# Kernel optimization log

Measured on AMD Instinct MI355X. Metric: run time of the kernel, lower is better.

## Reference

```python
import jax, jax.numpy as jnp
import numpy as np

N, M, CIN, COUT, K, KS = 200000, 100000, 32, 64, 32, 3


def setup_inputs() -> dict:
    key = jax.random.key(0)
    ks = jax.random.split(key, 6)
    inp_positions = jax.random.uniform(ks[0], (N, 3), dtype=jnp.float32)
    out_positions = jax.random.uniform(ks[1], (M, 3), dtype=jnp.float32)
    inp_features = jax.random.normal(ks[2], (N, CIN), dtype=jnp.float32)
    inp_importance = jnp.ones((N,), dtype=jnp.float32)
    neighbors_index = jax.random.randint(ks[3], (M, K), 0, N, dtype=jnp.int32)
    kernel = 0.05 * jax.random.normal(ks[4], (KS, KS, KS, CIN, COUT), dtype=jnp.float32)
    bias = jnp.zeros((COUT,), dtype=jnp.float32)
    extents = jnp.ones((1,), dtype=jnp.float32)
    return dict(inp_features=inp_features, inp_positions=inp_positions,
                out_positions=out_positions, extents=extents,
                inp_importance=inp_importance, neighbors_index=neighbors_index,
                kernel=kernel, bias=bias)


def _axis_weights(x):
    """x: [...,] coord clamped to [0, KS-1]. Returns [..., KS] linear interp weights."""
    grid = jnp.arange(KS, dtype=x.dtype)
    return jnp.maximum(0.0, 1.0 - jnp.abs(x[..., None] - grid))


def reference(inp_features, inp_positions, out_positions, extents,
              inp_importance, neighbors_index, kernel, bias):
    radius = 0.5 * extents[0]
    nbr_pos = inp_positions[neighbors_index]                   # [M,K,3]
    rel = (nbr_pos - out_positions[:, None, :]) / radius       # unit-ball coords
    dist = jnp.sqrt(jnp.sum(rel * rel, axis=-1))               # [M,K] L2 metric
    mask = (dist <= 1.0).astype(inp_features.dtype)            # in-radius validity
    # ball_to_cube_radial: scale radially so sphere boundary -> cube boundary
    linf = jnp.max(jnp.abs(rel), axis=-1)                      # [M,K]
    scale = jnp.where(linf > 1e-8, dist / jnp.maximum(linf, 1e-8), 0.0)
    cube = rel * scale[..., None]                              # in [-1,1]^3
    # align_corners=True: map [-1,1] to voxel-center coords [0, KS-1]
    coords = jnp.clip((cube + 1.0) * (0.5 * (KS - 1)), 0.0, KS - 1.0)  # 'linear' clamp
    wx = _axis_weights(coords[..., 0])                         # [M,K,3]
    wy = _axis_weights(coords[..., 1])
    wz = _axis_weights(coords[..., 2])
    imp = mask * inp_importance[neighbors_index]               # [M,K]
    feat = inp_features[neighbors_index] * imp[..., None]      # [M,K,CIN]
    # accumulate importance*interp-weighted features per filter voxel
    acc = jnp.einsum('mka,mkb,mkc,mki->mabci', wx, wy, wz, feat)  # [M,3,3,3,CIN]
    out = jnp.einsum('mabci,abcio->mo', acc, kernel)           # [M,COUT]
    # normalize=True, no window fn -> divide by (importance-weighted) neighbor count
    norm = jnp.sum(imp, axis=1)                                # [M]
    out = out * jnp.where(norm > 0, 1.0 / jnp.maximum(norm, 1e-12), 0.0)[:, None]
    return out + bias  # activation=None
```

## Files before the change

kernel.cpp:

```cpp
#include <hip/hip_runtime.h>


typedef __attribute__((ext_vector_type(8))) __bf16 bf16x8;
typedef __attribute__((ext_vector_type(4))) __bf16 bf16x4;
typedef __attribute__((ext_vector_type(4))) float f32x4;

constexpr int MPTS = 100000;
constexpr int MB   = 8;
constexpr int NBLK = MPTS / MB;

constexpr int PT_STRIDE = 2240;
constexpr int W_V       = 80;
constexpr int NRM_OFF   = MB * PT_STRIDE;
constexpr int LDS_BYTES = NRM_OFF + 32 + 304;

__global__ void wprep_kernel(const float* __restrict__ kern, __bf16* __restrict__ wsb) {
    const int tid = blockIdx.x * 256 + threadIdx.x;
    if (tid >= 4 * 28 * 64 * 8) return;
    const int j  = tid & 7;
    const int l  = (tid >> 3) & 63;
    const int s  = tid >> 9;
    const int ks = s % 28;
    const int nt = s / 28;
    const int kk = ks * 32 + ((l >> 4) << 3) + j;
    const int ch = kk / 28;
    const int v  = kk - ch * 28;
    const int o  = nt * 16 + (l & 15);
    const float val = (v < 27) ? kern[v * 2048 + ch * 64 + o] : 0.0f;
    wsb[tid] = (__bf16)val;
}

#define STAGE(f, A, B) do {                                              \
    f[0]  = feats[(size_t)(A).x * 32 + lr];                              \
    f[1]  = feats[(size_t)(A).y * 32 + lr];                              \
    f[2]  = feats[(size_t)(A).z * 32 + lr];                              \
    f[3]  = feats[(size_t)(A).w * 32 + lr];                              \
    f[4]  = feats[(size_t)(B).x * 32 + lr];                              \
    f[5]  = feats[(size_t)(B).y * 32 + lr];                              \
    f[6]  = feats[(size_t)(B).z * 32 + lr];                              \
    f[7]  = feats[(size_t)(B).w * 32 + lr];                              \
    f[8]  = feats[(size_t)(A).x * 32 + 16 + lr];                         \
    f[9]  = feats[(size_t)(A).y * 32 + 16 + lr];                         \
    f[10] = feats[(size_t)(A).z * 32 + 16 + lr];                         \
    f[11] = feats[(size_t)(A).w * 32 + 16 + lr];                         \
    f[12] = feats[(size_t)(B).x * 32 + 16 + lr];                         \
    f[13] = feats[(size_t)(B).y * 32 + 16 + lr];                         \
    f[14] = feats[(size_t)(B).z * 32 + 16 + lr];                         \
    f[15] = feats[(size_t)(B).w * 32 + 16 + lr];                         \
} while (0)

#define COMPUTE(qq, f) do {                                              \
    unsigned char* pbase = smem + (wv * 4 + (qq)) * PT_STRIDE;           \
    bf16x8 b0, b1;                                                       \
    b0[0] = (__bf16)f[0];  b0[1] = (__bf16)f[1];                         \
    b0[2] = (__bf16)f[2];  b0[3] = (__bf16)f[3];                         \
    b0[4] = (__bf16)f[4];  b0[5] = (__bf16)f[5];                         \
    b0[6] = (__bf16)f[6];  b0[7] = (__bf16)f[7];                         \
    b1[0] = (__bf16)f[8];  b1[1] = (__bf16)f[9];                         \
    b1[2] = (__bf16)f[10]; b1[3] = (__bf16)f[11];                        \
    b1[4] = (__bf16)f[12]; b1[5] = (__bf16)f[13];                        \
    b1[6] = (__bf16)f[14]; b1[7] = (__bf16)f[15];                        \
    const bf16x8 a0 = *(const bf16x8*)(pbase + lr * W_V + k0 * 2);       \
    const bf16x8 a1 = *(const bf16x8*)(pbase + (16 + lr) * W_V + k0 * 2);\
    f32x4 d00 = {0.f,0.f,0.f,0.f}, d01 = {0.f,0.f,0.f,0.f};              \
    f32x4 d10 = {0.f,0.f,0.f,0.f}, d11 = {0.f,0.f,0.f,0.f};              \
    d00 = __builtin_amdgcn_mfma_f32_16x16x32_bf16(a0, b0, d00, 0, 0, 0); \
    d01 = __builtin_amdgcn_mfma_f32_16x16x32_bf16(a0, b1, d01, 0, 0, 0); \
    d10 = __builtin_amdgcn_mfma_f32_16x16x32_bf16(a1, b0, d10, 0, 0, 0); \
    d11 = __builtin_amdgcn_mfma_f32_16x16x32_bf16(a1, b1, d11, 0, 0, 0); \
    const int vb0 = grp * 4, vb1 = 16 + grp * 4;                         \
    bf16x4 t0, t1;                                                       \
    t0[0] = (__bf16)d00[0]; t0[1] = (__bf16)d00[1];                      \
    t0[2] = (__bf16)d00[2]; t0[3] = (__bf16)d00[3];                      \
    *(bf16x4*)(pbase + (lr * 28 + vb0) * 2) = t0;                        \
    t1[0] = (__bf16)d01[0]; t1[1] = (__bf16)d01[1];                      \
    t1[2] = (__bf16)d01[2]; t1[3] = (__bf16)d01[3];                      \
    *(bf16x4*)(pbase + ((16 + lr) * 28 + vb0) * 2) = t1;                 \
    if (vb1 < 28) {                                                      \
        bf16x4 t2, t3;                                                   \
        t2[0] = (__bf16)d10[0]; t2[1] = (__bf16)d10[1];                  \
        t2[2] = (__bf16)d10[2]; t2[3] = (__bf16)d10[3];                  \
        *(bf16x4*)(pbase + (lr * 28 + vb1) * 2) = t2;                    \
        t3[0] = (__bf16)d11[0]; t3[1] = (__bf16)d11[1];                  \
        t3[2] = (__bf16)d11[2]; t3[3] = (__bf16)d11[3];                  \
        *(bf16x4*)(pbase + ((16 + lr) * 28 + vb1) * 2) = t3;             \
    }                                                                    \
} while (0)

__global__ __launch_bounds__(128, 4)
void cconv_kernel(const float* __restrict__ feats,
                  const float* __restrict__ inpos,
                  const float* __restrict__ outpos,
                  const float* __restrict__ extents,
                  const float* __restrict__ importance,
                  const int*   __restrict__ nbrs,
                  const __bf16* __restrict__ wfrag,
                  const float* __restrict__ bias,
                  float* __restrict__ out)
{
    __shared__ __align__(16) unsigned char smem[LDS_BYTES];

    const int tid = threadIdx.x;
    const int blk = blockIdx.x;
    float* nrm = (float*)(smem + NRM_OFF);

    const float inv_r = 2.0f / extents[0];

    {
        const int pt = tid >> 4;
        const int kp = tid & 15;
        const int m  = blk * MB + pt;
        const int2 nn = *(const int2*)(nbrs + m * 32 + 2 * kp);
        const float ox = outpos[3 * m + 0];
        const float oy = outpos[3 * m + 1];
        const float oz = outpos[3 * m + 2];

        float cxA, cyA, czA, impA, cxB, cyB, czB, impB;
        {
            const int nb = nn.x;
            const float rx = (inpos[3 * nb + 0] - ox) * inv_r;
            const float ry = (inpos[3 * nb + 1] - oy) * inv_r;
            const float rz = (inpos[3 * nb + 2] - oz) * inv_r;
            const float dist = sqrtf(rx * rx + ry * ry + rz * rz);
            float imp = importance[nb];
            impA = (dist <= 1.0f) ? imp : 0.0f;
            const float linf = fmaxf(fabsf(rx), fmaxf(fabsf(ry), fabsf(rz)));
            const float sc = (linf > 1e-8f) ? (dist / linf) : 0.0f;
            cxA = fminf(fmaxf(rx * sc + 1.0f, 0.0f), 2.0f);
            cyA = fminf(fmaxf(ry * sc + 1.0f, 0.0f), 2.0f);
            czA = fminf(fmaxf(rz * sc + 1.0f, 0.0f), 2.0f);
        }
        {
            const int nb = nn.y;
            const float rx = (inpos[3 * nb + 0] - ox) * inv_r;
            const float ry = (inpos[3 * nb + 1] - oy) * inv_r;
            const float rz = (inpos[3 * nb + 2] - oz) * inv_r;
            const float dist = sqrtf(rx * rx + ry * ry + rz * rz);
            float imp = importance[nb];
            impB = (dist <= 1.0f) ? imp : 0.0f;
            const float linf = fmaxf(fabsf(rx), fmaxf(fabsf(ry), fabsf(rz)));
            const float sc = (linf > 1e-8f) ? (dist / linf) : 0.0f;
            cxB = fminf(fmaxf(rx * sc + 1.0f, 0.0f), 2.0f);
            cyB = fminf(fmaxf(ry * sc + 1.0f, 0.0f), 2.0f);
            czB = fminf(fmaxf(rz * sc + 1.0f, 0.0f), 2.0f);
        }

        float wxA[3], wyA[3], wzA[3], wxB[3], wyB[3], wzB[3];
        wxA[0] = fmaxf(0.f, 1.f - cxA) * impA;
        wxA[1] = (1.f - fabsf(cxA - 1.f)) * impA;
        wxA[2] = fmaxf(0.f, cxA - 1.f) * impA;
        wyA[0] = fmaxf(0.f, 1.f - cyA); wyA[1] = 1.f - fabsf(cyA - 1.f); wyA[2] = fmaxf(0.f, cyA - 1.f);
        wzA[0] = fmaxf(0.f, 1.f - czA); wzA[1] = 1.f - fabsf(czA - 1.f); wzA[2] = fmaxf(0.f, czA - 1.f);
        wxB[0] = fmaxf(0.f, 1.f - cxB) * impB;
        wxB[1] = (1.f - fabsf(cxB - 1.f)) * impB;
        wxB[2] = fmaxf(0.f, cxB - 1.f) * impB;
        wyB[0] = fmaxf(0.f, 1.f - cyB); wyB[1] = 1.f - fabsf(cyB - 1.f); wyB[2] = fmaxf(0.f, cyB - 1.f);
        wzB[0] = fmaxf(0.f, 1.f - czB); wzB[1] = 1.f - fabsf(czB - 1.f); wzB[2] = fmaxf(0.f, czB - 1.f);

        unsigned char* wrow = smem + pt * PT_STRIDE + kp * 4;
#pragma unroll
        for (int a = 0; a < 3; ++a)
#pragma unroll
            for (int b = 0; b < 3; ++b) {
                const float pA = wxA[a] * wyA[b];
                const float pB = wxB[a] * wyB[b];
#pragma unroll
                for (int c = 0; c < 3; ++c) {
                    const int v = a * 9 + b * 3 + c;
                    union { __bf16 h[2]; unsigned int u; } pk;
                    pk.h[0] = (__bf16)(pA * wzA[c]);
                    pk.h[1] = (__bf16)(pB * wzB[c]);
                    *(unsigned int*)(wrow + v * W_V) = pk.u;
                }
            }
        *(unsigned int*)(wrow + 27 * W_V) = 0u;

        float s = impA + impB;
        s += __shfl_xor(s, 1);
        s += __shfl_xor(s, 2);
        s += __shfl_xor(s, 4);
        s += __shfl_xor(s, 8);
        if (kp == 0) nrm[pt] = (s > 0.f) ? (1.f / fmaxf(s, 1e-12f)) : 0.f;
    }

    const int wv   = tid >> 6;
    const int lane = tid & 63;
    const int grp  = lane >> 4;
    const int lr   = lane & 15;
    const int k0   = grp * 8;
    const int* nb_base = nbrs + (blk * MB + wv * 4) * 32 + k0;

    float f0[16], f1[16];
    {
        const int4 nA0 = *(const int4*)(nb_base);
        const int4 nB0 = *(const int4*)(nb_base + 4);
        STAGE(f0, nA0, nB0);
        const int4 nA1 = *(const int4*)(nb_base + 32);
        const int4 nB1 = *(const int4*)(nb_base + 36);
        STAGE(f1, nA1, nB1);
        COMPUTE(0, f0);
        const int4 nA2 = *(const int4*)(nb_base + 64);
        const int4 nB2 = *(const int4*)(nb_base + 68);
        STAGE(f0, nA2, nB2);
        COMPUTE(1, f1);
        const int4 nA3 = *(const int4*)(nb_base + 96);
        const int4 nB3 = *(const int4*)(nb_base + 100);
        STAGE(f1, nA3, nB3);
        COMPUTE(2, f0);
        COMPUTE(3, f1);
    }
    __syncthreads();

    const int nt0 = wv * 2, nt1 = wv * 2 + 1;
    const bf16x8* wb = (const bf16x8*)wfrag;
    const unsigned char* abase = smem + (lr & 7) * PT_STRIDE + grp * 16;

    f32x4 e0 = {0.f, 0.f, 0.f, 0.f}, e1 = {0.f, 0.f, 0.f, 0.f};
    bf16x8 w0c = wb[(nt0 * 28) * 64 + lane];
    bf16x8 w1c = wb[(nt1 * 28) * 64 + lane];
    bf16x8 ac  = *(const bf16x8*)(abase);
#pragma unroll
    for (int ks = 0; ks < 28; ++ks) {
        if (ks < 27) {
            const bf16x8 w0n = wb[(nt0 * 28 + ks + 1) * 64 + lane];
            const bf16x8 w1n = wb[(nt1 * 28 + ks + 1) * 64 + lane];
            const bf16x8 an  = *(const bf16x8*)(abase + (ks + 1) * 64);
            e0 = __builtin_amdgcn_mfma_f32_16x16x32_bf16(ac, w0c, e0, 0, 0, 0);
            e1 = __builtin_amdgcn_mfma_f32_16x16x32_bf16(ac, w1c, e1, 0, 0, 0);
            w0c = w0n; w1c = w1n; ac = an;
        } else {
            e0 = __builtin_amdgcn_mfma_f32_16x16x32_bf16(ac, w0c, e0, 0, 0, 0);
            e1 = __builtin_amdgcn_mfma_f32_16x16x32_bf16(ac, w1c, e1, 0, 0, 0);
        }
    }

    const int o0 = nt0 * 16 + lr;
    const int o1 = nt1 * 16 + lr;
    const float bb0 = bias[o0];
    const float bb1 = bias[o1];
    if (grp < 2) {
#pragma unroll
        for (int r = 0; r < 4; ++r) {
            const int pt = grp * 4 + r;
            const float nv = nrm[pt];
            const int mg = blk * MB + pt;
            out[mg * 64 + o0] = e0[r] * nv + bb0;
            out[mg * 64 + o1] = e1[r] * nv + bb1;
        }
    }
}

extern "C" void kernel_launch(void* const* d_in, const int* in_sizes, int n_in,
                              void* d_out, int out_size, void* d_ws, size_t ws_size,
                              hipStream_t stream) {
    (void)in_sizes; (void)n_in; (void)out_size; (void)ws_size;
    const float* feats      = (const float*)d_in[0];
    const float* inpos      = (const float*)d_in[1];
    const float* outpos     = (const float*)d_in[2];
    const float* extents    = (const float*)d_in[3];
    const float* importance = (const float*)d_in[4];
    const int*   nbrs       = (const int*)d_in[5];
    const float* kern       = (const float*)d_in[6];
    const float* bias       = (const float*)d_in[7];
    float* outp = (float*)d_out;
    __bf16* wsb = (__bf16*)d_ws;

    hipLaunchKernelGGL(wprep_kernel, dim3(224), dim3(256), 0, stream, kern, wsb);
    hipLaunchKernelGGL(cconv_kernel, dim3(NBLK), dim3(128), 0, stream,
                       feats, inpos, outpos, extents, importance,
                       nbrs, wsb, bias, outp);
}
```

Baseline: 210.8 us.

## Pre-convert features to bf16 and widen block to 16 points

Adds a prep pass that converts the whole input feature table to bf16 in workspace, so the gather loads half as many bytes per neighbour as packed channel pairs. The conv block grows from 8 to 16 output points and 256 threads, with each wave owning one output tile and a double-buffered weight prefetch in the second GEMM. All four stages are issued before compute, which raises register pressure, and the prep pass adds a full read and write of the feature table on every call. A fallback to fp32 float2 gathers is kept for when the workspace is too small.

```diff
diff --git a/kernel.cpp b/kernel.cpp
--- a/kernel.cpp
+++ b/kernel.cpp
@@ -4,91 +4,126 @@
 typedef __attribute__((ext_vector_type(8))) __bf16 bf16x8;
 typedef __attribute__((ext_vector_type(4))) __bf16 bf16x4;
 typedef __attribute__((ext_vector_type(4))) float f32x4;
-
+typedef unsigned int u32;
+typedef unsigned short u16;
+
+constexpr int NPTS = 200000;
 constexpr int MPTS = 100000;
-constexpr int MB   = 8;
+constexpr int MB   = 16;
 constexpr int NBLK = MPTS / MB;
 
-constexpr int PT_STRIDE = 2240;
+constexpr int PT_STRIDE = 2256;
 constexpr int W_V       = 80;
 constexpr int NRM_OFF   = MB * PT_STRIDE;
-constexpr int LDS_BYTES = NRM_OFF + 32 + 304;
-
-__global__ void wprep_kernel(const float* __restrict__ kern, __bf16* __restrict__ wsb) {
-    const int tid = blockIdx.x * 256 + threadIdx.x;
-    if (tid >= 4 * 28 * 64 * 8) return;
-    const int j  = tid & 7;
-    const int l  = (tid >> 3) & 63;
-    const int s  = tid >> 9;
-    const int ks = s % 28;
-    const int nt = s / 28;
-    const int kk = ks * 32 + ((l >> 4) << 3) + j;
-    const int ch = kk / 28;
-    const int v  = kk - ch * 28;
-    const int o  = nt * 16 + (l & 15);
-    const float val = (v < 27) ? kern[v * 2048 + ch * 64 + o] : 0.0f;
-    wsb[tid] = (__bf16)val;
+constexpr int LDS_BYTES = NRM_OFF + 64 + 256;
+
+constexpr size_t WFRAG_ELEMS = 4 * 28 * 64 * 8;
+constexpr size_t FEATS_OFF_ELEMS = WFRAG_ELEMS;
+constexpr size_t WS_NEED = (WFRAG_ELEMS + (size_t)NPTS * 32) * 2;
+
+__global__ void prep_kernel(const float* __restrict__ kern,
+                            const float* __restrict__ feats,
+                            __bf16* __restrict__ wsb) {
+    const int blk = blockIdx.x;
+    if (blk < 224) {
+        const int tid = blk * 256 + threadIdx.x;
+        const int j  = tid & 7;
+        const int l  = (tid >> 3) & 63;
+        const int s  = tid >> 9;
+        const int ks = s % 28;
+        const int nt = s / 28;
+        const int kk = ks * 32 + ((l >> 4) << 3) + j;
+        const int ch = kk / 28;
+        const int v  = kk - ch * 28;
+        const int o  = nt * 16 + (l & 15);
+        const float val = (v < 27) ? kern[v * 2048 + ch * 64 + o] : 0.0f;
+        wsb[tid] = (__bf16)val;
+    } else {
+        const int t = (blk - 224) * 256 + threadIdx.x;
+        const float4* src = (const float4*)feats + (size_t)t * 2;
+        const float4 a = src[0];
+        const float4 b = src[1];
+        bf16x8 o;
+        o[0]=(__bf16)a.x; o[1]=(__bf16)a.y; o[2]=(__bf16)a.z; o[3]=(__bf16)a.w;
+        o[4]=(__bf16)b.x; o[5]=(__bf16)b.y; o[6]=(__bf16)b.z; o[7]=(__bf16)b.w;
+        *(bf16x8*)(wsb + FEATS_OFF_ELEMS + (size_t)t * 8) = o;
+    }
 }
 
-#define STAGE(f, A, B) do {                                              \
-    f[0]  = feats[(size_t)(A).x * 32 + lr];                              \
-    f[1]  = feats[(size_t)(A).y * 32 + lr];                              \
-    f[2]  = feats[(size_t)(A).z * 32 + lr];                              \
-    f[3]  = feats[(size_t)(A).w * 32 + lr];                              \
-    f[4]  = feats[(size_t)(B).x * 32 + lr];                              \
-    f[5]  = feats[(size_t)(B).y * 32 + lr];                              \
-    f[6]  = feats[(size_t)(B).z * 32 + lr];                              \
-    f[7]  = feats[(size_t)(B).w * 32 + lr];                              \
-    f[8]  = feats[(size_t)(A).x * 32 + 16 + lr];                         \
-    f[9]  = feats[(size_t)(A).y * 32 + 16 + lr];                         \
-    f[10] = feats[(size_t)(A).z * 32 + 16 + lr];                         \
-    f[11] = feats[(size_t)(A).w * 32 + 16 + lr];                         \
-    f[12] = feats[(size_t)(B).x * 32 + 16 + lr];                         \
-    f[13] = feats[(size_t)(B).y * 32 + 16 + lr];                         \
-    f[14] = feats[(size_t)(B).z * 32 + 16 + lr];                         \
-    f[15] = feats[(size_t)(B).w * 32 + 16 + lr];                         \
+#define STAGE(q) do {                                                       \
+    const int4 nA = *(const int4*)(nb_base + (q) * 32);                     \
+    const int4 nB = *(const int4*)(nb_base + (q) * 32 + 4);                 \
+    if constexpr (PRE) {                                                    \
+        stq[q][0] = featsb[(size_t)nA.x * 16 + lr];                         \
+        stq[q][1] = featsb[(size_t)nA.y * 16 + lr];                         \
+        stq[q][2] = featsb[(size_t)nA.z * 16 + lr];                         \
+        stq[q][3] = featsb[(size_t)nA.w * 16 + lr];                         \
+        stq[q][4] = featsb[(size_t)nB.x * 16 + lr];                         \
+        stq[q][5] = featsb[(size_t)nB.y * 16 + lr];                         \
+        stq[q][6] = featsb[(size_t)nB.z * 16 + lr];                         \
+        stq[q][7] = featsb[(size_t)nB.w * 16 + lr];                         \
+    } else {                                                                \
+        stf[q][0] = ((const float2*)(feats + (size_t)nA.x * 32))[lr];       \
+        stf[q][1] = ((const float2*)(feats + (size_t)nA.y * 32))[lr];       \
+        stf[q][2] = ((const float2*)(feats + (size_t)nA.z * 32))[lr];       \
+        stf[q][3] = ((const float2*)(feats + (size_t)nA.w * 32))[lr];       \
+        stf[q][4] = ((const float2*)(feats + (size_t)nB.x * 32))[lr];       \
+        stf[q][5] = ((const float2*)(feats + (size_t)nB.y * 32))[lr];       \
+        stf[q][6] = ((const float2*)(feats + (size_t)nB.z * 32))[lr];       \
+        stf[q][7] = ((const float2*)(feats + (size_t)nB.w * 32))[lr];       \
+    }                                                                       \
 } while (0)
 
-#define COMPUTE(qq, f) do {                                              \
-    unsigned char* pbase = smem + (wv * 4 + (qq)) * PT_STRIDE;           \
-    bf16x8 b0, b1;                                                       \
-    b0[0] = (__bf16)f[0];  b0[1] = (__bf16)f[1];                         \
-    b0[2] = (__bf16)f[2];  b0[3] = (__bf16)f[3];                         \
-    b0[4] = (__bf16)f[4];  b0[5] = (__bf16)f[5];                         \
-    b0[6] = (__bf16)f[6];  b0[7] = (__bf16)f[7];                         \
-    b1[0] = (__bf16)f[8];  b1[1] = (__bf16)f[9];                         \
-    b1[2] = (__bf16)f[10]; b1[3] = (__bf16)f[11];                        \
-    b1[4] = (__bf16)f[12]; b1[5] = (__bf16)f[13];                        \
-    b1[6] = (__bf16)f[14]; b1[7] = (__bf16)f[15];                        \
-    const bf16x8 a0 = *(const bf16x8*)(pbase + lr * W_V + k0 * 2);       \
-    const bf16x8 a1 = *(const bf16x8*)(pbase + (16 + lr) * W_V + k0 * 2);\
-    f32x4 d00 = {0.f,0.f,0.f,0.f}, d01 = {0.f,0.f,0.f,0.f};              \
-    f32x4 d10 = {0.f,0.f,0.f,0.f}, d11 = {0.f,0.f,0.f,0.f};              \
-    d00 = __builtin_amdgcn_mfma_f32_16x16x32_bf16(a0, b0, d00, 0, 0, 0); \
-    d01 = __builtin_amdgcn_mfma_f32_16x16x32_bf16(a0, b1, d01, 0, 0, 0); \
-    d10 = __builtin_amdgcn_mfma_f32_16x16x32_bf16(a1, b0, d10, 0, 0, 0); \
-    d11 = __builtin_amdgcn_mfma_f32_16x16x32_bf16(a1, b1, d11, 0, 0, 0); \
-    const int vb0 = grp * 4, vb1 = 16 + grp * 4;                         \
-    bf16x4 t0, t1;                                                       \
-    t0[0] = (__bf16)d00[0]; t0[1] = (__bf16)d00[1];                      \
-    t0[2] = (__bf16)d00[2]; t0[3] = (__bf16)d00[3];                      \
-    *(bf16x4*)(pbase + (lr * 28 + vb0) * 2) = t0;                        \
-    t1[0] = (__bf16)d01[0]; t1[1] = (__bf16)d01[1];                      \
-    t1[2] = (__bf16)d01[2]; t1[3] = (__bf16)d01[3];                      \
-    *(bf16x4*)(pbase + ((16 + lr) * 28 + vb0) * 2) = t1;                 \
-    if (vb1 < 28) {                                                      \
-        bf16x4 t2, t3;                                                   \
-        t2[0] = (__bf16)d10[0]; t2[1] = (__bf16)d10[1];                  \
-        t2[2] = (__bf16)d10[2]; t2[3] = (__bf16)d10[3];                  \
-        *(bf16x4*)(pbase + (lr * 28 + vb1) * 2) = t2;                    \
-        t3[0] = (__bf16)d11[0]; t3[1] = (__bf16)d11[1];                  \
-        t3[2] = (__bf16)d11[2]; t3[3] = (__bf16)d11[3];                  \
-        *(bf16x4*)(pbase + ((16 + lr) * 28 + vb1) * 2) = t3;             \
-    }                                                                    \
+#define COMPUTE(q) do {                                                     \
+    unsigned char* pbase = smem + (wv * 4 + (q)) * PT_STRIDE;               \
+    bf16x8 b0, b1;                                                          \
+    if constexpr (PRE) {                                                    \
+        union { u16 u[8]; bf16x8 v; } B0, B1;                               \
+        _Pragma("unroll")                                                   \
+        for (int j = 0; j < 8; ++j) {                                       \
+            B0.u[j] = (u16)(stq[q][j] & 0xffffu);                           \
+            B1.u[j] = (u16)(stq[q][j] >> 16);                               \
+        }                                                                   \
+        b0 = B0.v; b1 = B1.v;                                               \
+    } else {                                                                \
+        _Pragma("unroll")                                                   \
+        for (int j = 0; j < 8; ++j) {                                       \
+            b0[j] = (__bf16)stf[q][j].x;                                    \
+            b1[j] = (__bf16)stf[q][j].y;                                    \
+        }                                                                   \
+    }                                                                       \
+    const bf16x8 a0 = *(const bf16x8*)(pbase + lr * W_V + k0 * 2);          \
+    const bf16x8 a1 = *(const bf16x8*)(pbase + (16 + lr) * W_V + k0 * 2);   \
+    f32x4 d00 = {0.f,0.f,0.f,0.f}, d01 = {0.f,0.f,0.f,0.f};                 \
+    f32x4 d10 = {0.f,0.f,0.f,0.f}, d11 = {0.f,0.f,0.f,0.f};                 \
+    d00 = __builtin_amdgcn_mfma_f32_16x16x32_bf16(a0, b0, d00, 0, 0, 0);    \
+    d01 = __builtin_amdgcn_mfma_f32_16x16x32_bf16(a0, b1, d01, 0, 0, 0);    \
+    d10 = __builtin_amdgcn_mfma_f32_16x16x32_bf16(a1, b0, d10, 0, 0, 0);    \
+    d11 = __builtin_amdgcn_mfma_f32_16x16x32_bf16(a1, b1, d11, 0, 0, 0);    \
+    const int vb0 = grp * 4, vb1 = 16 + grp * 4;                            \
+    const int ch0 = 2 * lr, ch1 = 2 * lr + 1;                               \
+    bf16x4 t0, t1;                                                          \
+    t0[0]=(__bf16)d00[0]; t0[1]=(__bf16)d00[1];                             \
+    t0[2]=(__bf16)d00[2]; t0[3]=(__bf16)d00[3];                             \
+    *(bf16x4*)(pbase + (ch0 * 28 + vb0) * 2) = t0;                          \
+    t1[0]=(__bf16)d01[0]; t1[1]=(__bf16)d01[1];                             \
+    t1[2]=(__bf16)d01[2]; t1[3]=(__bf16)d01[3];                             \
+    *(bf16x4*)(pbase + (ch1 * 28 + vb0) * 2) = t1;                          \
+    if (vb1 < 28) {                                                         \
+        bf16x4 t2, t3;                                                      \
+        t2[0]=(__bf16)d10[0]; t2[1]=(__bf16)d10[1];                         \
+        t2[2]=(__bf16)d10[2]; t2[3]=(__bf16)d10[3];                         \
+        *(bf16x4*)(pbase + (ch0 * 28 + vb1) * 2) = t2;                      \
+        t3[0]=(__bf16)d11[0]; t3[1]=(__bf16)d11[1];                         \
+        t3[2]=(__bf16)d11[2]; t3[3]=(__bf16)d11[3];                         \
+        *(bf16x4*)(pbase + (ch1 * 28 + vb1) * 2) = t3;                      \
+    }                                                                       \
 } while (0)
 
-__global__ __launch_bounds__(128, 4)
+template<bool PRE>
+__global__ __launch_bounds__(256, 4)
 void cconv_kernel(const float* __restrict__ feats,
+                  const u32* __restrict__ featsb,
                   const float* __restrict__ inpos,
                   const float* __restrict__ outpos,
                   const float* __restrict__ extents,
@@ -167,13 +202,13 @@
 #pragma unroll
                 for (int c = 0; c < 3; ++c) {
                     const int v = a * 9 + b * 3 + c;
-                    union { __bf16 h[2]; unsigned int u; } pk;
+                    union { __bf16 h[2]; u32 u; } pk;
                     pk.h[0] = (__bf16)(pA * wzA[c]);
                     pk.h[1] = (__bf16)(pB * wzB[c]);
-                    *(unsigned int*)(wrow + v * W_V) = pk.u;
+                    *(u32*)(wrow + v * W_V) = pk.u;
                 }
             }
-        *(unsigned int*)(wrow + 27 * W_V) = 0u;
+        *(u32*)(wrow + 27 * W_V) = 0u;
 
         float s = impA + impB;
         s += __shfl_xor(s, 1);
@@ -190,70 +225,43 @@
     const int k0   = grp * 8;
     const int* nb_base = nbrs + (blk * MB + wv * 4) * 32 + k0;
 
-    float f0[16], f1[16];
-    {
-        const int4 nA0 = *(const int4*)(nb_base);
-        const int4 nB0 = *(const int4*)(nb_base + 4);
-        STAGE(f0, nA0, nB0);
-        const int4 nA1 = *(const int4*)(nb_base + 32);
-        const int4 nB1 = *(const int4*)(nb_base + 36);
-        STAGE(f1, nA1, nB1);
-        COMPUTE(0, f0);
-        const int4 nA2 = *(const int4*)(nb_base + 64);
-        const int4 nB2 = *(const int4*)(nb_base + 68);
-        STAGE(f0, nA2, nB2);
-        COMPUTE(1, f1);
-        const int4 nA3 = *(const int4*)(nb_base + 96);
-        const int4 nB3 = *(const int4*)(nb_base + 100);
-        STAGE(f1, nA3, nB3);
-        COMPUTE(2, f0);
-        COMPUTE(3, f1);
-    }
+    u32    stq[4][8];
+    float2 stf[4][8];
+    STAGE(0); STAGE(1); STAGE(2); STAGE(3);
+    COMPUTE(0); COMPUTE(1); COMPUTE(2); COMPUTE(3);
+
+    const bf16x8* wb = (const bf16x8*)wfrag;
+    bf16x8 w0 = wb[(size_t)(wv * 28 + 0) * 64 + lane];
+    bf16x8 w1 = wb[(size_t)(wv * 28 + 1) * 64 + lane];
     __syncthreads();
 
-    const int nt0 = wv * 2, nt1 = wv * 2 + 1;
-    const bf16x8* wb = (const bf16x8*)wfrag;
-    const unsigned char* abase = smem + (lr & 7) * PT_STRIDE + grp * 16;
-
-    f32x4 e0 = {0.f, 0.f, 0.f, 0.f}, e1 = {0.f, 0.f, 0.f, 0.f};
-    bf16x8 w0c = wb[(nt0 * 28) * 64 + lane];
-    bf16x8 w1c = wb[(nt1 * 28) * 64 + lane];
-    bf16x8 ac  = *(const bf16x8*)(abase);
+    const unsigned char* abase = smem + lr * PT_STRIDE + grp * 16;
+    f32x4 e = {0.f, 0.f, 0.f, 0.f};
+    bf16x8 a = *(const bf16x8*)(abase);
 #pragma unroll
     for (int ks = 0; ks < 28; ++ks) {
-        if (ks < 27) {
-            const bf16x8 w0n = wb[(nt0 * 28 + ks + 1) * 64 + lane];
-            const bf16x8 w1n = wb[(nt1 * 28 + ks + 1) * 64 + lane];
-            const bf16x8 an  = *(const bf16x8*)(abase + (ks + 1) * 64);
-            e0 = __builtin_amdgcn_mfma_f32_16x16x32_bf16(ac, w0c, e0, 0, 0, 0);
-            e1 = __builtin_amdgcn_mfma_f32_16x16x32_bf16(ac, w1c, e1, 0, 0, 0);
-            w0c = w0n; w1c = w1n; ac = an;
-        } else {
-            e0 = __builtin_amdgcn_mfma_f32_16x16x32_bf16(ac, w0c, e0, 0, 0, 0);
-            e1 = __builtin_amdgcn_mfma_f32_16x16x32_bf16(ac, w1c, e1, 0, 0, 0);
-        }
-    }
-
-    const int o0 = nt0 * 16 + lr;
-    const int o1 = nt1 * 16 + lr;
-    const float bb0 = bias[o0];
-    const float bb1 = bias[o1];
-    if (grp < 2) {
-#pragma unroll
-        for (int r = 0; r < 4; ++r) {
-            const int pt = grp * 4 + r;
-            const float nv = nrm[pt];
-            const int mg = blk * MB + pt;
-            out[mg * 64 + o0] = e0[r] * nv + bb0;
-            out[mg * 64 + o1] = e1[r] * nv + bb1;
-        }
+        bf16x8 wn, an;
+        if (ks < 26) wn = wb[(size_t)(wv * 28 + ks + 2) * 64 + lane];
+        if (ks < 27) an = *(const bf16x8*)(abase + (ks + 1) * 64);
+        e = __builtin_amdgcn_mfma_f32_16x16x32_bf16(a, w0, e, 0, 0, 0);
+        w0 = w1;
+        if (ks < 26) w1 = wn;
+        if (ks < 27) a = an;
+    }
+
+    const int o  = wv * 16 + lr;
+    const float bb = bias[o];
+#pragma unroll
+    for (int r = 0; r < 4; ++r) {
+        const int pt = grp * 4 + r;
+        out[(size_t)(blk * MB + pt) * 64 + o] = e[r] * nrm[pt] + bb;
     }
 }
 
 extern "C" void kernel_launch(void* const* d_in, const int* in_sizes, int n_in,
                               void* d_out, int out_size, void* d_ws, size_t ws_size,
                               hipStream_t stream) {
-    (void)in_sizes; (void)n_in; (void)out_size; (void)ws_size;
+    (void)in_sizes; (void)n_in; (void)out_size;
     const float* feats      = (const float*)d_in[0];
     const float* inpos      = (const float*)d_in[1];
     const float* outpos     = (const float*)d_in[2];
@@ -265,8 +273,17 @@
     float* outp = (float*)d_out;
     __bf16* wsb = (__bf16*)d_ws;
 
-    hipLaunchKernelGGL(wprep_kernel, dim3(224), dim3(256), 0, stream, kern, wsb);
-    hipLaunchKernelGGL(cconv_kernel, dim3(NBLK), dim3(128), 0, stream,
-                       feats, inpos, outpos, extents, importance,
-                       nbrs, wsb, bias, outp);
+    const bool pre = ws_size >= WS_NEED;
+
+    hipLaunchKernelGGL(prep_kernel, dim3(pre ? 3349 : 224), dim3(256), 0, stream,
+                       kern, feats, wsb);
+    if (pre) {
+        hipLaunchKernelGGL(cconv_kernel<true>, dim3(NBLK), dim3(256), 0, stream,
+                           feats, (const u32*)(wsb + FEATS_OFF_ELEMS), inpos, outpos,
+                           extents, importance, nbrs, wsb, bias, outp);
+    } else {
+        hipLaunchKernelGGL(cconv_kernel<false>, dim3(NBLK), dim3(256), 0, stream,
+                           feats, (const u32*)(wsb + FEATS_OFF_ELEMS), inpos, outpos,
+                           extents, importance, nbrs, wsb, bias, outp);
+    }
 }
```

Result: faster. 189.7 us (-10.0%).
